# Kernel optimization log

Measured on AMD Instinct MI355X. Metric: run time of the kernel, lower is better.

The kernel has to match this reference:

```python
import jax, jax.numpy as jnp
import numpy as np

ALPHA = 0.2  # leaky_relu negative slope
NEG_INF = -9e15


def gat_layer(h_in, W, a, adj_mask):
    """One GATLayer (eval mode, dropout disabled).
    h_in: [N, F_in], W: [F_in, F_out], a: [2*F_out, 1], adj_mask: [N, N] bool.
    Equivalent to the torch repeat/cat construction: e_ij = leaky_relu(a1.h_i + a2.h_j).
    """
    h = h_in @ W                          # [N, F_out]
    F_out = W.shape[1]
    a1 = a[:F_out, 0]                     # [F_out]
    a2 = a[F_out:, 0]                     # [F_out]
    f1 = h @ a1                           # [N]
    f2 = h @ a2                           # [N]
    e = jax.nn.leaky_relu(f1[:, None] + f2[None, :], negative_slope=ALPHA)  # [N, N]
    e = jnp.where(adj_mask, e, NEG_INF)
    attn = jax.nn.softmax(e, axis=-1)     # rows sum to 1
    return jax.nn.elu(attn @ h)           # [N, F_out]


def setup_inputs() -> dict:
    key = jax.random.key(0)
    ks = jax.random.split(key, 6)
    N, F_in, F_hid, F_out, H = 8192, 29, 8, 2, 4
    x = jax.random.normal(ks[0], (N, F_in), dtype=jnp.float32)
    adj = jax.random.randint(ks[1], (N, N), 0, 2, dtype=jnp.int32)
    # xavier_uniform with gain=1.414
    def xavier(k, shape, gain=1.414):
        fan_in, fan_out = shape[0], shape[1]
        bound = gain * np.sqrt(6.0 / (fan_in + fan_out))
        return jax.random.uniform(k, shape, jnp.float32, -bound, bound)
    W_heads = jnp.stack([xavier(k, (F_in, F_hid)) for k in jax.random.split(ks[2], H)])   # [H, 29, 8]
    a_heads = jnp.stack([xavier(k, (2 * F_hid, 1)) for k in jax.random.split(ks[3], H)])  # [H, 16, 1]
    W_out = xavier(ks[4], (F_hid * H, F_out))   # [32, 2]
    a_out = xavier(ks[5], (2 * F_out, 1))       # [4, 1]
    return {"x": x, "adj": adj, "W_heads": W_heads, "a_heads": a_heads,
            "W_out": W_out, "a_out": a_out}


def reference(x, adj, W_heads, a_heads, W_out, a_out):
    adj_mask = adj > 0
    heads = jax.vmap(lambda W, a: gat_layer(x, W, a, adj_mask))(W_heads, a_heads)  # [H, N, 8]
    hcat = jnp.concatenate(list(heads), axis=1)   # [N, H*8] (same order as torch cat over heads)
    out = gat_layer(hcat, W_out, a_out, adj_mask)  # [N, 2]
    return jax.nn.log_softmax(out, axis=1)
```

## Files before the change

### kernel.cpp

```cpp
#include <hip/hip_runtime.h>
#include <math.h>

#define N 8192
#define NW 128
#define FIN 29
#define FH 8
#define NH 4
#define ALPHA 0.2f
#define LOG2E 1.4426950408889634f
#define JS 4
#define JRR (N / JS)
#define JS2 4

typedef unsigned long long ull;
typedef unsigned short u16;
typedef __attribute__((ext_vector_type(8))) short bf16x8;
typedef __attribute__((ext_vector_type(4))) float f32x4;

__device__ inline unsigned bf16rn(float f) {
    unsigned u = __float_as_uint(f);
    return (u + 0x7fffu + ((u >> 16) & 1u)) >> 16;
}
__device__ inline unsigned fenc(float x) {
    unsigned u = __float_as_uint(x);
    return (u & 0x80000000u) ? ~u : (u | 0x80000000u);
}
__device__ inline float fdec(unsigned e) {
    return __uint_as_float((e & 0x80000000u) ? (e & 0x7fffffffu) : ~e);
}

__global__ void k0_pack(const int* __restrict__ adj, ull* __restrict__ mask,
                        unsigned* __restrict__ amax) {
    int row = blockIdx.x;
    int tid = threadIdx.x;
    int lane = tid & 63;
    int wave = tid >> 6;
    if (row == 0 && tid < 8) amax[tid] = 0u;
    const int* rp = adj + (size_t)row * N;
#pragma unroll 8
    for (int i = 0; i < 32; i++) {
        int a = rp[i * 256 + tid];
        ull b = __ballot(a > 0);
        if (lane == 0) mask[(size_t)row * NW + i * 4 + wave] = b;
    }
}

__global__ __launch_bounds__(256) void k1_feat(
    const float* __restrict__ x, const float* __restrict__ Wh,
    const float* __restrict__ ah,
    float2* __restrict__ e2, u16* __restrict__ Bpk,
    float* __restrict__ f1a, unsigned* __restrict__ amax) {
    __shared__ float sx[64 * FIN];
    __shared__ float sW[NH * FIN * FH];
    __shared__ float sa[NH * 2 * FH];
    int tid = threadIdx.x;
    for (int i = tid; i < NH * FIN * FH; i += 256) sW[i] = Wh[i];
    for (int i = tid; i < NH * 2 * FH; i += 256) sa[i] = ah[i];
    for (int i = tid; i < 64 * FIN; i += 256) sx[i] = x[(size_t)blockIdx.x * 64 * FIN + i];
    __syncthreads();
    int h = tid & 3;
    int nl = tid >> 2;
    int node = blockIdx.x * 64 + nl;
    float hv[FH];
#pragma unroll
    for (int k = 0; k < FH; k++) {
        float s = 0.f;
#pragma unroll
        for (int f = 0; f < FIN; f++) s += sx[nl * FIN + f] * sW[(h * FIN + f) * FH + k];
        hv[k] = s;
    }
    float f1 = 0.f, f2 = 0.f;
#pragma unroll
    for (int k = 0; k < FH; k++) {
        f1 += hv[k] * sa[h * 16 + k];
        f2 += hv[k] * sa[h * 16 + 8 + k];
    }
    float f1L = f1 * LOG2E, f2L = f2 * LOG2E;
    f1a[node * 4 + h] = f1L;
    e2[(size_t)h * N + node] = make_float2(__builtin_amdgcn_exp2f(f2L),
                                           __builtin_amdgcn_exp2f(ALPHA * f2L));
    int js = node >> 11;
    int t  = (node >> 6) & 31;
    int hfl = (node >> 5) & 1;
    int kb = (node >> 3) & 3;
    int e  = node & 7;
    u16* dst = Bpk + ((size_t)(((h * 4 + js) * 32 + t) * 2 + hfl)) * 512 + e;
#pragma unroll
    for (int cc = 0; cc < 16; cc++) {
        u16 v = (cc < FH) ? (u16)bf16rn(hv[cc])
                          : ((cc == 8) ? (u16)0x3F80u : (u16)0);
        dst[(kb * 16 + cc) * 8] = v;
    }
    float v = f2L;
    for (int off = 4; off < 64; off <<= 1) v = fmaxf(v, __shfl_xor(v, off, 64));
    if ((tid & 63) < 4) atomicMax(&amax[tid & 3], fenc(v));
}

__global__ __launch_bounds__(256, 4) void k3_attn1(
    const ull* __restrict__ mask, const float2* __restrict__ e2,
    const uint4* __restrict__ Bpk, const float* __restrict__ f1a,
    const unsigned* __restrict__ amax, float* __restrict__ part1) {
    int tid = threadIdx.x;
    int lane = tid & 63;
    int wave = tid >> 6;
    int h = blockIdx.x & 3;
    int js = (blockIdx.x >> 2) & 3;
    int rowblk = blockIdx.x >> 4;
    int jbase = js * JRR;

    int c = lane & 15;
    int kb = lane >> 4;
    int sh = kb * 8;
    int r0 = rowblk * 128 + wave * 16 + c;
    int r1 = r0 + 64;

    float mfL = fdec(amax[h]);
    float f1 = f1a[r0 * 4 + h];
    float vv = f1 + mfL, mm = fmaxf(vv, ALPHA * vv);
    float e1p0 = __builtin_amdgcn_exp2f(f1 - mm);
    float e1n0 = __builtin_amdgcn_exp2f(ALPHA * f1 - mm);
    f1 = f1a[r1 * 4 + h];
    vv = f1 + mfL; mm = fmaxf(vv, ALPHA * vv);
    float e1p1 = __builtin_amdgcn_exp2f(f1 - mm);
    float e1n1 = __builtin_amdgcn_exp2f(ALPHA * f1 - mm);

    const ull* mr0 = mask + (size_t)r0 * NW + (jbase >> 6);
    const ull* mr1 = mask + (size_t)r1 * NW + (jbase >> 6);
    const float2* e2h = e2 + (size_t)h * N + jbase + kb * 8;
    const uint4* bp0 = Bpk + (size_t)(h * 4 + js) * 4096 + lane;

    f32x4 acc0 = {0.f, 0.f, 0.f, 0.f};
    f32x4 acc1 = {0.f, 0.f, 0.f, 0.f};

    for (int t = 0; t < JRR / 64; t++) {
        ull mw0 = mr0[t];
        ull mw1 = mr1[t];
#pragma unroll
        for (int hf = 0; hf < 2; hf++) {
            const float4* qp = (const float4*)(e2h + t * 64 + hf * 32);
            float4 q0 = qp[0], q1 = qp[1], q2 = qp[2], q3 = qp[3];
            uint4 bp = bp0[(t * 2 + hf) * 64];
            unsigned sw0 = ((unsigned)(mw0 >> (hf * 32))) >> sh;
            unsigned sw1 = ((unsigned)(mw1 >> (hf * 32))) >> sh;
            {
                float w0 = fmaxf(e1p0 * q0.x, e1n0 * q0.y);
                float w1 = fmaxf(e1p0 * q0.z, e1n0 * q0.w);
                float w2 = fmaxf(e1p0 * q1.x, e1n0 * q1.y);
                float w3 = fmaxf(e1p0 * q1.z, e1n0 * q1.w);
                float w4 = fmaxf(e1p0 * q2.x, e1n0 * q2.y);
                float w5 = fmaxf(e1p0 * q2.z, e1n0 * q2.w);
                float w6 = fmaxf(e1p0 * q3.x, e1n0 * q3.y);
                float w7 = fmaxf(e1p0 * q3.z, e1n0 * q3.w);
                w0 = (sw0 & 1u)   ? w0 : 0.f;
                w1 = (sw0 & 2u)   ? w1 : 0.f;
                w2 = (sw0 & 4u)   ? w2 : 0.f;
                w3 = (sw0 & 8u)   ? w3 : 0.f;
                w4 = (sw0 & 16u)  ? w4 : 0.f;
                w5 = (sw0 & 32u)  ? w5 : 0.f;
                w6 = (sw0 & 64u)  ? w6 : 0.f;
                w7 = (sw0 & 128u) ? w7 : 0.f;
                uint4 ap;
                asm("v_cvt_pk_bf16_f32 %0, %1, %2" : "=v"(ap.x) : "v"(w0), "v"(w1));
                asm("v_cvt_pk_bf16_f32 %0, %1, %2" : "=v"(ap.y) : "v"(w2), "v"(w3));
                asm("v_cvt_pk_bf16_f32 %0, %1, %2" : "=v"(ap.z) : "v"(w4), "v"(w5));
                asm("v_cvt_pk_bf16_f32 %0, %1, %2" : "=v"(ap.w) : "v"(w6), "v"(w7));
                acc0 = __builtin_amdgcn_mfma_f32_16x16x32_bf16(
                    __builtin_bit_cast(bf16x8, ap), __builtin_bit_cast(bf16x8, bp),
                    acc0, 0, 0, 0);
            }
            {
                float w0 = fmaxf(e1p1 * q0.x, e1n1 * q0.y);
                float w1 = fmaxf(e1p1 * q0.z, e1n1 * q0.w);
                float w2 = fmaxf(e1p1 * q1.x, e1n1 * q1.y);
                float w3 = fmaxf(e1p1 * q1.z, e1n1 * q1.w);
                float w4 = fmaxf(e1p1 * q2.x, e1n1 * q2.y);
                float w5 = fmaxf(e1p1 * q2.z, e1n1 * q2.w);
                float w6 = fmaxf(e1p1 * q3.x, e1n1 * q3.y);
                float w7 = fmaxf(e1p1 * q3.z, e1n1 * q3.w);
                w0 = (sw1 & 1u)   ? w0 : 0.f;
                w1 = (sw1 & 2u)   ? w1 : 0.f;
                w2 = (sw1 & 4u)   ? w2 : 0.f;
                w3 = (sw1 & 8u)   ? w3 : 0.f;
                w4 = (sw1 & 16u)  ? w4 : 0.f;
                w5 = (sw1 & 32u)  ? w5 : 0.f;
                w6 = (sw1 & 64u)  ? w6 : 0.f;
                w7 = (sw1 & 128u) ? w7 : 0.f;
                uint4 ap;
                asm("v_cvt_pk_bf16_f32 %0, %1, %2" : "=v"(ap.x) : "v"(w0), "v"(w1));
                asm("v_cvt_pk_bf16_f32 %0, %1, %2" : "=v"(ap.y) : "v"(w2), "v"(w3));
                asm("v_cvt_pk_bf16_f32 %0, %1, %2" : "=v"(ap.z) : "v"(w4), "v"(w5));
                asm("v_cvt_pk_bf16_f32 %0, %1, %2" : "=v"(ap.w) : "v"(w6), "v"(w7));
                acc1 = __builtin_amdgcn_mfma_f32_16x16x32_bf16(
                    __builtin_bit_cast(bf16x8, ap), __builtin_bit_cast(bf16x8, bp),
                    acc1, 0, 0, 0);
            }
        }
    }
    if (c <= 8) {
        int ro = rowblk * 128 + wave * 16 + kb * 4;
        float* dst = part1 + (size_t)(js * 36 + h * 9 + c) * N + ro;
        *(float4*)dst = make_float4(acc0[0], acc0[1], acc0[2], acc0[3]);
        *(float4*)(dst + 64) = make_float4(acc1[0], acc1[1], acc1[2], acc1[3]);
    }
}

__global__ void k3b_final(const float* __restrict__ part1, const float* __restrict__ Wo,
                          const float* __restrict__ ao,
                          float4* __restrict__ rec2, float* __restrict__ f1b,
                          unsigned* __restrict__ amax) {
    __shared__ float sW[64];
    __shared__ float sa[4];
    int tid = threadIdx.x;
    if (tid < 64) sW[tid] = Wo[tid];
    if (tid < 4) sa[tid] = ao[tid];
    __syncthreads();
    int row = blockIdx.x * 256 + tid;
    float hv[32];
#pragma unroll
    for (int h = 0; h < NH; h++) {
        float s[9];
#pragma unroll
        for (int cc = 0; cc < 9; cc++) {
            float acc = 0.f;
#pragma unroll
            for (int js = 0; js < JS; js++)
                acc += part1[(size_t)(js * 36 + h * 9 + cc) * N + row];
            s[cc] = acc;
        }
        float inv = 1.f / s[8];
#pragma unroll
        for (int k = 0; k < FH; k++) {
            float o = s[k] * inv;
            hv[h * 8 + k] = (o > 0.f) ? o : expm1f(o);
        }
    }
    float h0 = 0.f, h1 = 0.f;
#pragma unroll
    for (int i = 0; i < 32; i++) {
        h0 = fmaf(hv[i], sW[i * 2 + 0], h0);
        h1 = fmaf(hv[i], sW[i * 2 + 1], h1);
    }
    float f1 = (h0 * sa[0] + h1 * sa[1]) * LOG2E;
    float f2 = (h0 * sa[2] + h1 * sa[3]) * LOG2E;
    rec2[row] = make_float4(__builtin_amdgcn_exp2f(f2), h0, h1,
                            __builtin_amdgcn_exp2f(ALPHA * f2));
    f1b[row] = f1;
    float vmax = f2;
    for (int off = 32; off > 0; off >>= 1) vmax = fmaxf(vmax, __shfl_xor(vmax, off, 64));
    if ((tid & 63) == 0) atomicMax(&amax[4], fenc(vmax));
}

__global__ __launch_bounds__(256) void k6_attn2(
    const ull* __restrict__ mask, const float4* __restrict__ rec2,
    const float* __restrict__ f1b, const unsigned* __restrict__ amax,
    float* __restrict__ part2) {
    int tid = threadIdx.x;
    int lane = tid & 63;
    int wave = tid >> 6;
    int blk = blockIdx.x >> 2;
    int js = blockIdx.x & 3;
    int rbase = blk * 16 + wave * 4;
    const int JR = N / JS2;
    int jbase = js * JR;

    float mb = fdec(amax[4]);
    float e1p[4], e1n[4];
#pragma unroll
    for (int i = 0; i < 4; i++) {
        float f1 = f1b[rbase + i];
        float v = f1 + mb, m = fmaxf(v, ALPHA * v);
        e1p[i] = __builtin_amdgcn_exp2f(f1 - m);
        e1n[i] = __builtin_amdgcn_exp2f(ALPHA * f1 - m);
    }
    float a0[4] = {0.f, 0.f, 0.f, 0.f};
    float a1[4] = {0.f, 0.f, 0.f, 0.f};
    float dd[4] = {0.f, 0.f, 0.f, 0.f};
    const ull* mr[4];
#pragma unroll
    for (int i = 0; i < 4; i++) mr[i] = mask + (size_t)(rbase + i) * NW;

    int wb = jbase >> 6;
#pragma unroll 4
    for (int s = 0; s < JR / 64; s++) {
        float4 q = rec2[jbase + s * 64 + lane];
#pragma unroll
        for (int i = 0; i < 4; i++) {
            ull mw = mr[i][wb + s];
            float w = fmaxf(e1p[i] * q.x, e1n[i] * q.w);
            w = ((mw >> lane) & 1ull) ? w : 0.f;
            a0[i] = fmaf(w, q.y, a0[i]);
            a1[i] = fmaf(w, q.z, a1[i]);
            dd[i] += w;
        }
    }
#pragma unroll
    for (int i = 0; i < 4; i++) {
        for (int off = 32; off > 0; off >>= 1) {
            a0[i] += __shfl_xor(a0[i], off, 64);
            a1[i] += __shfl_xor(a1[i], off, 64);
            dd[i] += __shfl_xor(dd[i], off, 64);
        }
    }
    if (lane == 0) {
#pragma unroll
        for (int i = 0; i < 4; i++) {
            int row = rbase + i;
            part2[(js * 3 + 0) * N + row] = a0[i];
            part2[(js * 3 + 1) * N + row] = a1[i];
            part2[(js * 3 + 2) * N + row] = dd[i];
        }
    }
}

__global__ void k6b_final(const float* __restrict__ part2, float* __restrict__ out) {
    int row = blockIdx.x * 256 + threadIdx.x;
    float s0 = 0.f, s1 = 0.f, d = 0.f;
#pragma unroll
    for (int js = 0; js < JS2; js++) {
        s0 += part2[(js * 3 + 0) * N + row];
        s1 += part2[(js * 3 + 1) * N + row];
        d  += part2[(js * 3 + 2) * N + row];
    }
    float inv = 1.f / d;
    float e0 = s0 * inv, e1 = s1 * inv;
    e0 = (e0 > 0.f) ? e0 : expm1f(e0);
    e1 = (e1 > 0.f) ? e1 : expm1f(e1);
    float mx = fmaxf(e0, e1);
    float lse = mx + logf(expf(e0 - mx) + expf(e1 - mx));
    ((float2*)out)[row] = make_float2(e0 - lse, e1 - lse);
}

extern "C" void kernel_launch(void* const* d_in, const int* in_sizes, int n_in,
                              void* d_out, int out_size, void* d_ws, size_t ws_size,
                              hipStream_t stream) {
    const float* x   = (const float*)d_in[0];
    const int*   adj = (const int*)d_in[1];
    const float* Wh  = (const float*)d_in[2];
    const float* ah  = (const float*)d_in[3];
    const float* Wo  = (const float*)d_in[4];
    const float* ao  = (const float*)d_in[5];
    float* out = (float*)d_out;
    float* ws = (float*)d_ws;

    ull*      mask  = (ull*)ws;
    float2*   e2    = (float2*)(ws + 2097152);
    u16*      Bpk   = (u16*)(ws + 2162688);
    float*    f1a   = ws + 2424832;
    float*    part1 = ws + 2457600;
    float4*   rec2  = (float4*)(ws + 3637248);
    float*    f1b   = ws + 3670016;
    float*    part2 = ws + 3678208;
    unsigned* amax  = (unsigned*)(ws + 3776512);

    k0_pack<<<N, 256, 0, stream>>>(adj, mask, amax);
    k1_feat<<<N / 64, 256, 0, stream>>>(x, Wh, ah, e2, Bpk, f1a, amax);
    k3_attn1<<<(N / 128) * JS * NH, 256, 0, stream>>>(mask, e2, (const uint4*)Bpk, f1a, amax, part1);
    k3b_final<<<N / 256, 256, 0, stream>>>(part1, Wo, ao, rec2, f1b, amax);
    k6_attn2<<<(N / 16) * JS2, 256, 0, stream>>>(mask, rec2, f1b, amax, part2);
    k6b_final<<<N / 256, 256, 0, stream>>>(part2, out);
}
```

Measured before the change: 503.9 us.

## Transpose adjacency bitmask, split exp tables, pack muls, fuse final layer-2 reduction

Adds a kernel that transposes the packed adjacency bitmask so attention kernels read mask words for consecutive rows with coalesced loads instead of strided per-row reads. The exp(f2) table is split into separate positive/negative arrays, which lets the weight computation use packed v_pk_mul_f32. The second attention kernel drops its j-split and the separate final kernel, handling the full row per wave and applying ELU/log_softmax directly. This costs an extra transpose pass and workspace, and the layer-2 kernel now runs with fewer, longer blocks.

New measurement: 514.7 us. 1.02x slower.

```diff
diff --git a/kernel.cpp b/kernel.cpp
--- a/kernel.cpp
+++ b/kernel.cpp
@@ -10,12 +10,12 @@
 #define LOG2E 1.4426950408889634f
 #define JS 4
 #define JRR (N / JS)
-#define JS2 4
 
 typedef unsigned long long ull;
 typedef unsigned short u16;
 typedef __attribute__((ext_vector_type(8))) short bf16x8;
 typedef __attribute__((ext_vector_type(4))) float f32x4;
+typedef __attribute__((ext_vector_type(2))) float f32x2;
 
 __device__ inline unsigned bf16rn(float f) {
     unsigned u = __float_as_uint(f);
@@ -27,6 +27,11 @@
 }
 __device__ inline float fdec(unsigned e) {
     return __uint_as_float((e & 0x80000000u) ? (e & 0x7fffffffu) : ~e);
+}
+__device__ inline f32x2 pk_mul(f32x2 a, f32x2 b) {
+    f32x2 d;
+    asm("v_pk_mul_f32 %0, %1, %2" : "=v"(d) : "v"(a), "v"(b));
+    return d;
 }
 
 __global__ void k0_pack(const int* __restrict__ adj, ull* __restrict__ mask,
@@ -45,10 +50,31 @@
     }
 }
 
+__global__ __launch_bounds__(256) void k0t_transpose(
+    const ull* __restrict__ mask, ull* __restrict__ maskT) {
+    __shared__ ull sT[64][65];
+    int tid = threadIdx.x;
+    int ln = tid & 63;
+    int wv = tid >> 6;
+    int br = blockIdx.x >> 1;
+    int bw = blockIdx.x & 1;
+#pragma unroll
+    for (int i = 0; i < 16; i++) {
+        int rr = i * 4 + wv;
+        sT[rr][ln] = mask[(size_t)(br * 64 + rr) * NW + bw * 64 + ln];
+    }
+    __syncthreads();
+#pragma unroll
+    for (int i = 0; i < 16; i++) {
+        int ww = i * 4 + wv;
+        maskT[(size_t)(bw * 64 + ww) * N + br * 64 + ln] = sT[ln][ww];
+    }
+}
+
 __global__ __launch_bounds__(256) void k1_feat(
     const float* __restrict__ x, const float* __restrict__ Wh,
     const float* __restrict__ ah,
-    float2* __restrict__ e2, u16* __restrict__ Bpk,
+    float* __restrict__ e2p, float* __restrict__ e2n, u16* __restrict__ Bpk,
     float* __restrict__ f1a, unsigned* __restrict__ amax) {
     __shared__ float sx[64 * FIN];
     __shared__ float sW[NH * FIN * FH];
@@ -77,8 +103,8 @@
     }
     float f1L = f1 * LOG2E, f2L = f2 * LOG2E;
     f1a[node * 4 + h] = f1L;
-    e2[(size_t)h * N + node] = make_float2(__builtin_amdgcn_exp2f(f2L),
-                                           __builtin_amdgcn_exp2f(ALPHA * f2L));
+    e2p[(size_t)h * N + node] = __builtin_amdgcn_exp2f(f2L);
+    e2n[(size_t)h * N + node] = __builtin_amdgcn_exp2f(ALPHA * f2L);
     int js = node >> 11;
     int t  = (node >> 6) & 31;
     int hfl = (node >> 5) & 1;
@@ -96,10 +122,41 @@
     if ((tid & 63) < 4) atomicMax(&amax[tid & 3], fenc(v));
 }
 
+#define WTILE(E1P2, E1N2, SW, ACC)                                              \
+    {                                                                           \
+        f32x2 wp, wn;                                                           \
+        float w0, w1, w2, w3, w4, w5, w6, w7;                                   \
+        wp = pk_mul(E1P2, p01); wn = pk_mul(E1N2, n01);                         \
+        w0 = fmaxf(wp[0], wn[0]); w1 = fmaxf(wp[1], wn[1]);                     \
+        wp = pk_mul(E1P2, p23); wn = pk_mul(E1N2, n23);                         \
+        w2 = fmaxf(wp[0], wn[0]); w3 = fmaxf(wp[1], wn[1]);                     \
+        wp = pk_mul(E1P2, p45); wn = pk_mul(E1N2, n45);                         \
+        w4 = fmaxf(wp[0], wn[0]); w5 = fmaxf(wp[1], wn[1]);                     \
+        wp = pk_mul(E1P2, p67); wn = pk_mul(E1N2, n67);                         \
+        w6 = fmaxf(wp[0], wn[0]); w7 = fmaxf(wp[1], wn[1]);                     \
+        w0 = (SW & 1u)   ? w0 : 0.f;                                            \
+        w1 = (SW & 2u)   ? w1 : 0.f;                                            \
+        w2 = (SW & 4u)   ? w2 : 0.f;                                            \
+        w3 = (SW & 8u)   ? w3 : 0.f;                                            \
+        w4 = (SW & 16u)  ? w4 : 0.f;                                            \
+        w5 = (SW & 32u)  ? w5 : 0.f;                                            \
+        w6 = (SW & 64u)  ? w6 : 0.f;                                            \
+        w7 = (SW & 128u) ? w7 : 0.f;                                            \
+        uint4 ap;                                                               \
+        asm("v_cvt_pk_bf16_f32 %0, %1, %2" : "=v"(ap.x) : "v"(w0), "v"(w1));    \
+        asm("v_cvt_pk_bf16_f32 %0, %1, %2" : "=v"(ap.y) : "v"(w2), "v"(w3));    \
+        asm("v_cvt_pk_bf16_f32 %0, %1, %2" : "=v"(ap.z) : "v"(w4), "v"(w5));    \
+        asm("v_cvt_pk_bf16_f32 %0, %1, %2" : "=v"(ap.w) : "v"(w6), "v"(w7));    \
+        ACC = __builtin_amdgcn_mfma_f32_16x16x32_bf16(                          \
+            __builtin_bit_cast(bf16x8, ap), __builtin_bit_cast(bf16x8, bp),     \
+            ACC, 0, 0, 0);                                                      \
+    }
+
 __global__ __launch_bounds__(256, 4) void k3_attn1(
-    const ull* __restrict__ mask, const float2* __restrict__ e2,
-    const uint4* __restrict__ Bpk, const float* __restrict__ f1a,
-    const unsigned* __restrict__ amax, float* __restrict__ part1) {
+    const ull* __restrict__ maskT, const float* __restrict__ e2p,
+    const float* __restrict__ e2n, const uint4* __restrict__ Bpk,
+    const float* __restrict__ f1a, const unsigned* __restrict__ amax,
+    float* __restrict__ part1) {
     int tid = threadIdx.x;
     int lane = tid & 63;
     int wave = tid >> 6;
@@ -117,83 +174,44 @@
     float mfL = fdec(amax[h]);
     float f1 = f1a[r0 * 4 + h];
     float vv = f1 + mfL, mm = fmaxf(vv, ALPHA * vv);
-    float e1p0 = __builtin_amdgcn_exp2f(f1 - mm);
-    float e1n0 = __builtin_amdgcn_exp2f(ALPHA * f1 - mm);
+    f32x2 e1p0 = {0.f, 0.f}, e1n0 = {0.f, 0.f}, e1p1 = {0.f, 0.f}, e1n1 = {0.f, 0.f};
+    e1p0[0] = e1p0[1] = __builtin_amdgcn_exp2f(f1 - mm);
+    e1n0[0] = e1n0[1] = __builtin_amdgcn_exp2f(ALPHA * f1 - mm);
     f1 = f1a[r1 * 4 + h];
     vv = f1 + mfL; mm = fmaxf(vv, ALPHA * vv);
-    float e1p1 = __builtin_amdgcn_exp2f(f1 - mm);
-    float e1n1 = __builtin_amdgcn_exp2f(ALPHA * f1 - mm);
-
-    const ull* mr0 = mask + (size_t)r0 * NW + (jbase >> 6);
-    const ull* mr1 = mask + (size_t)r1 * NW + (jbase >> 6);
-    const float2* e2h = e2 + (size_t)h * N + jbase + kb * 8;
+    e1p1[0] = e1p1[1] = __builtin_amdgcn_exp2f(f1 - mm);
+    e1n1[0] = e1n1[1] = __builtin_amdgcn_exp2f(ALPHA * f1 - mm);
+
+    const ull* mT = maskT + (size_t)(jbase >> 6) * N;
+    const float* pph = e2p + (size_t)h * N + jbase + kb * 8;
+    const float* nnh = e2n + (size_t)h * N + jbase + kb * 8;
     const uint4* bp0 = Bpk + (size_t)(h * 4 + js) * 4096 + lane;
 
     f32x4 acc0 = {0.f, 0.f, 0.f, 0.f};
     f32x4 acc1 = {0.f, 0.f, 0.f, 0.f};
 
     for (int t = 0; t < JRR / 64; t++) {
-        ull mw0 = mr0[t];
-        ull mw1 = mr1[t];
+        ull mw0 = mT[(size_t)t * N + r0];
+        ull mw1 = mT[(size_t)t * N + r1];
 #pragma unroll
         for (int hf = 0; hf < 2; hf++) {
-            const float4* qp = (const float4*)(e2h + t * 64 + hf * 32);
-            float4 q0 = qp[0], q1 = qp[1], q2 = qp[2], q3 = qp[3];
+            f32x4 P0 = *(const f32x4*)(pph + t * 64 + hf * 32);
+            f32x4 P1 = *(const f32x4*)(pph + t * 64 + hf * 32 + 4);
+            f32x4 Q0 = *(const f32x4*)(nnh + t * 64 + hf * 32);
+            f32x4 Q1 = *(const f32x4*)(nnh + t * 64 + hf * 32 + 4);
+            f32x2 p01 = __builtin_shufflevector(P0, P0, 0, 1);
+            f32x2 p23 = __builtin_shufflevector(P0, P0, 2, 3);
+            f32x2 p45 = __builtin_shufflevector(P1, P1, 0, 1);
+            f32x2 p67 = __builtin_shufflevector(P1, P1, 2, 3);
+            f32x2 n01 = __builtin_shufflevector(Q0, Q0, 0, 1);
+            f32x2 n23 = __builtin_shufflevector(Q0, Q0, 2, 3);
+            f32x2 n45 = __builtin_shufflevector(Q1, Q1, 0, 1);
+            f32x2 n67 = __builtin_shufflevector(Q1, Q1, 2, 3);
             uint4 bp = bp0[(t * 2 + hf) * 64];
             unsigned sw0 = ((unsigned)(mw0 >> (hf * 32))) >> sh;
             unsigned sw1 = ((unsigned)(mw1 >> (hf * 32))) >> sh;
-            {
-                float w0 = fmaxf(e1p0 * q0.x, e1n0 * q0.y);
-                float w1 = fmaxf(e1p0 * q0.z, e1n0 * q0.w);
-                float w2 = fmaxf(e1p0 * q1.x, e1n0 * q1.y);
-                float w3 = fmaxf(e1p0 * q1.z, e1n0 * q1.w);
-                float w4 = fmaxf(e1p0 * q2.x, e1n0 * q2.y);
-                float w5 = fmaxf(e1p0 * q2.z, e1n0 * q2.w);
-                float w6 = fmaxf(e1p0 * q3.x, e1n0 * q3.y);
-                float w7 = fmaxf(e1p0 * q3.z, e1n0 * q3.w);
-                w0 = (sw0 & 1u)   ? w0 : 0.f;
-                w1 = (sw0 & 2u)   ? w1 : 0.f;
-                w2 = (sw0 & 4u)   ? w2 : 0.f;
-                w3 = (sw0 & 8u)   ? w3 : 0.f;
-                w4 = (sw0 & 16u)  ? w4 : 0.f;
-                w5 = (sw0 & 32u)  ? w5 : 0.f;
-                w6 = (sw0 & 64u)  ? w6 : 0.f;
-                w7 = (sw0 & 128u) ? w7 : 0.f;
-                uint4 ap;
-                asm("v_cvt_pk_bf16_f32 %0, %1, %2" : "=v"(ap.x) : "v"(w0), "v"(w1));
-                asm("v_cvt_pk_bf16_f32 %0, %1, %2" : "=v"(ap.y) : "v"(w2), "v"(w3));
-                asm("v_cvt_pk_bf16_f32 %0, %1, %2" : "=v"(ap.z) : "v"(w4), "v"(w5));
-                asm("v_cvt_pk_bf16_f32 %0, %1, %2" : "=v"(ap.w) : "v"(w6), "v"(w7));
-                acc0 = __builtin_amdgcn_mfma_f32_16x16x32_bf16(
-                    __builtin_bit_cast(bf16x8, ap), __builtin_bit_cast(bf16x8, bp),
-                    acc0, 0, 0, 0);
-            }
-            {
-                float w0 = fmaxf(e1p1 * q0.x, e1n1 * q0.y);
-                float w1 = fmaxf(e1p1 * q0.z, e1n1 * q0.w);
-                float w2 = fmaxf(e1p1 * q1.x, e1n1 * q1.y);
-                float w3 = fmaxf(e1p1 * q1.z, e1n1 * q1.w);
-                float w4 = fmaxf(e1p1 * q2.x, e1n1 * q2.y);
-                float w5 = fmaxf(e1p1 * q2.z, e1n1 * q2.w);
-                float w6 = fmaxf(e1p1 * q3.x, e1n1 * q3.y);
-                float w7 = fmaxf(e1p1 * q3.z, e1n1 * q3.w);
-                w0 = (sw1 & 1u)   ? w0 : 0.f;
-                w1 = (sw1 & 2u)   ? w1 : 0.f;
-                w2 = (sw1 & 4u)   ? w2 : 0.f;
-                w3 = (sw1 & 8u)   ? w3 : 0.f;
-                w4 = (sw1 & 16u)  ? w4 : 0.f;
-                w5 = (sw1 & 32u)  ? w5 : 0.f;
-                w6 = (sw1 & 64u)  ? w6 : 0.f;
-                w7 = (sw1 & 128u) ? w7 : 0.f;
-                uint4 ap;
-                asm("v_cvt_pk_bf16_f32 %0, %1, %2" : "=v"(ap.x) : "v"(w0), "v"(w1));
-                asm("v_cvt_pk_bf16_f32 %0, %1, %2" : "=v"(ap.y) : "v"(w2), "v"(w3));
-                asm("v_cvt_pk_bf16_f32 %0, %1, %2" : "=v"(ap.z) : "v"(w4), "v"(w5));
-                asm("v_cvt_pk_bf16_f32 %0, %1, %2" : "=v"(ap.w) : "v"(w6), "v"(w7));
-                acc1 = __builtin_amdgcn_mfma_f32_16x16x32_bf16(
-                    __builtin_bit_cast(bf16x8, ap), __builtin_bit_cast(bf16x8, bp),
-                    acc1, 0, 0, 0);
-            }
+            WTILE(e1p0, e1n0, sw0, acc0)
+            WTILE(e1p1, e1n1, sw1, acc1)
         }
     }
     if (c <= 8) {
@@ -251,83 +269,65 @@
 }
 
 __global__ __launch_bounds__(256) void k6_attn2(
-    const ull* __restrict__ mask, const float4* __restrict__ rec2,
+    const ull* __restrict__ maskT, const float4* __restrict__ rec2,
     const float* __restrict__ f1b, const unsigned* __restrict__ amax,
-    float* __restrict__ part2) {
+    float* __restrict__ out) {
     int tid = threadIdx.x;
     int lane = tid & 63;
     int wave = tid >> 6;
-    int blk = blockIdx.x >> 2;
-    int js = blockIdx.x & 3;
-    int rbase = blk * 16 + wave * 4;
-    const int JR = N / JS2;
-    int jbase = js * JR;
+    int r0 = blockIdx.x * 8 + wave * 2;
 
     float mb = fdec(amax[4]);
-    float e1p[4], e1n[4];
-#pragma unroll
-    for (int i = 0; i < 4; i++) {
-        float f1 = f1b[rbase + i];
-        float v = f1 + mb, m = fmaxf(v, ALPHA * v);
-        e1p[i] = __builtin_amdgcn_exp2f(f1 - m);
-        e1n[i] = __builtin_amdgcn_exp2f(ALPHA * f1 - m);
-    }
-    float a0[4] = {0.f, 0.f, 0.f, 0.f};
-    float a1[4] = {0.f, 0.f, 0.f, 0.f};
-    float dd[4] = {0.f, 0.f, 0.f, 0.f};
-    const ull* mr[4];
-#pragma unroll
-    for (int i = 0; i < 4; i++) mr[i] = mask + (size_t)(rbase + i) * NW;
-
-    int wb = jbase >> 6;
+    float f1 = f1b[r0];
+    float v = f1 + mb, m = fmaxf(v, ALPHA * v);
+    float e1p0 = __builtin_amdgcn_exp2f(f1 - m);
+    float e1n0 = __builtin_amdgcn_exp2f(ALPHA * f1 - m);
+    f1 = f1b[r0 + 1];
+    v = f1 + mb; m = fmaxf(v, ALPHA * v);
+    float e1p1 = __builtin_amdgcn_exp2f(f1 - m);
+    float e1n1 = __builtin_amdgcn_exp2f(ALPHA * f1 - m);
+
+    float a00 = 0.f, a10 = 0.f, d0 = 0.f;
+    float a01 = 0.f, a11 = 0.f, d1 = 0.f;
 #pragma unroll 4
-    for (int s = 0; s < JR / 64; s++) {
-        float4 q = rec2[jbase + s * 64 + lane];
-#pragma unroll
-        for (int i = 0; i < 4; i++) {
-            ull mw = mr[i][wb + s];
-            float w = fmaxf(e1p[i] * q.x, e1n[i] * q.w);
-            w = ((mw >> lane) & 1ull) ? w : 0.f;
-            a0[i] = fmaf(w, q.y, a0[i]);
-            a1[i] = fmaf(w, q.z, a1[i]);
-            dd[i] += w;
+    for (int s = 0; s < NW; s++) {
+        float4 q = rec2[s * 64 + lane];
+        ull mw0 = maskT[(size_t)s * N + r0];
+        ull mw1 = maskT[(size_t)s * N + r0 + 1];
+        float w0 = fmaxf(e1p0 * q.x, e1n0 * q.w);
+        w0 = ((mw0 >> lane) & 1ull) ? w0 : 0.f;
+        float w1 = fmaxf(e1p1 * q.x, e1n1 * q.w);
+        w1 = ((mw1 >> lane) & 1ull) ? w1 : 0.f;
+        a00 = fmaf(w0, q.y, a00);
+        a10 = fmaf(w0, q.z, a10);
+        d0 += w0;
+        a01 = fmaf(w1, q.y, a01);
+        a11 = fmaf(w1, q.z, a11);
+        d1 += w1;
+    }
+    for (int off = 32; off > 0; off >>= 1) {
+        a00 += __shfl_xor(a00, off, 64);
+        a10 += __shfl_xor(a10, off, 64);
+        d0  += __shfl_xor(d0,  off, 64);
+        a01 += __shfl_xor(a01, off, 64);
+        a11 += __shfl_xor(a11, off, 64);
+        d1  += __shfl_xor(d1,  off, 64);
+    }
+    if (lane == 0) {
+#pragma unroll
+        for (int i = 0; i < 2; i++) {
+            float s0 = i ? a01 : a00;
+            float s1 = i ? a11 : a10;
+            float dd = i ? d1 : d0;
+            float inv = 1.f / dd;
+            float e0 = s0 * inv, e1 = s1 * inv;
+            e0 = (e0 > 0.f) ? e0 : expm1f(e0);
+            e1 = (e1 > 0.f) ? e1 : expm1f(e1);
+            float mx = fmaxf(e0, e1);
+            float lse = mx + logf(expf(e0 - mx) + expf(e1 - mx));
+            ((float2*)out)[r0 + i] = make_float2(e0 - lse, e1 - lse);
         }
     }
-#pragma unroll
-    for (int i = 0; i < 4; i++) {
-        for (int off = 32; off > 0; off >>= 1) {
-            a0[i] += __shfl_xor(a0[i], off, 64);
-            a1[i] += __shfl_xor(a1[i], off, 64);
-            dd[i] += __shfl_xor(dd[i], off, 64);
-        }
-    }
-    if (lane == 0) {
-#pragma unroll
-        for (int i = 0; i < 4; i++) {
-            int row = rbase + i;
-            part2[(js * 3 + 0) * N + row] = a0[i];
-            part2[(js * 3 + 1) * N + row] = a1[i];
-            part2[(js * 3 + 2) * N + row] = dd[i];
-        }
-    }
-}
-
-__global__ void k6b_final(const float* __restrict__ part2, float* __restrict__ out) {
-    int row = blockIdx.x * 256 + threadIdx.x;
-    float s0 = 0.f, s1 = 0.f, d = 0.f;
-#pragma unroll
-    for (int js = 0; js < JS2; js++) {
-        s0 += part2[(js * 3 + 0) * N + row];
-        s1 += part2[(js * 3 + 1) * N + row];
-        d  += part2[(js * 3 + 2) * N + row];
-    }
-    float inv = 1.f / d;
-    float e0 = s0 * inv, e1 = s1 * inv;
-    e0 = (e0 > 0.f) ? e0 : expm1f(e0);
-    e1 = (e1 > 0.f) ? e1 : expm1f(e1);
-    float mx = fmaxf(e0, e1);
-    float lse = mx + logf(expf(e0 - mx) + expf(e1 - mx));
-    ((float2*)out)[row] = make_float2(e0 - lse, e1 - lse);
 }
 
 extern "C" void kernel_launch(void* const* d_in, const int* in_sizes, int n_in,
@@ -343,19 +343,21 @@
     float* ws = (float*)d_ws;
 
     ull*      mask  = (ull*)ws;
-    float2*   e2    = (float2*)(ws + 2097152);
-    u16*      Bpk   = (u16*)(ws + 2162688);
-    float*    f1a   = ws + 2424832;
-    float*    part1 = ws + 2457600;
-    float4*   rec2  = (float4*)(ws + 3637248);
-    float*    f1b   = ws + 3670016;
-    float*    part2 = ws + 3678208;
-    unsigned* amax  = (unsigned*)(ws + 3776512);
+    ull*      maskT = (ull*)(ws + 2097152);
+    float*    e2p   = ws + 4194304;
+    float*    e2n   = ws + 4227072;
+    u16*      Bpk   = (u16*)(ws + 4259840);
+    float*    f1a   = ws + 4521984;
+    float*    part1 = ws + 4554752;
+    float4*   rec2  = (float4*)(ws + 5734400);
+    float*    f1b   = ws + 5767168;
+    unsigned* amax  = (unsigned*)(ws + 5775360);
 
     k0_pack<<<N, 256, 0, stream>>>(adj, mask, amax);
-    k1_feat<<<N / 64, 256, 0, stream>>>(x, Wh, ah, e2, Bpk, f1a, amax);
-    k3_attn1<<<(N / 128) * JS * NH, 256, 0, stream>>>(mask, e2, (const uint4*)Bpk, f1a, amax, part1);
+    k0t_transpose<<<256, 256, 0, stream>>>(mask, maskT);
+    k1_feat<<<N / 64, 256, 0, stream>>>(x, Wh, ah, e2p, e2n, Bpk, f1a, amax);
+    k3_attn1<<<(N / 128) * JS * NH, 256, 0, stream>>>(maskT, e2p, e2n, (const uint4*)Bpk,
+                                                      f1a, amax, part1);
     k3b_final<<<N / 256, 256, 0, stream>>>(part1, Wo, ao, rec2, f1b, amax);
-    k6_attn2<<<(N / 16) * JS2, 256, 0, stream>>>(mask, rec2, f1b, amax, part2);
-    k6b_final<<<N / 256, 256, 0, stream>>>(part2, out);
-}
+    k6_attn2<<<N / 8, 256, 0, stream>>>(maskT, rec2, f1b, amax, out);
+}
```
